# Performance work log

Hardware: AMD Instinct MI355X
Metric: run time of the kernel (lower is better)

The kernel has to match this reference:

```python
import jax, jax.numpy as jnp
import numpy as np

B, S, D_DIM = 32, 512, 1024

def setup_inputs() -> dict:
    key = jax.random.key(0)
    k1, k2, k3, k4 = jax.random.split(key, 4)
    return {
        "D": jax.random.normal(k1, (B, S, D_DIM), dtype=jnp.float32),
        "H": jax.random.normal(k2, (B, S, D_DIM), dtype=jnp.float32),
        # learned params: U is (d+1, d) (xavier-style scale), W is (2d+1,)
        # (original inits W to zeros; we use small random values so the linear
        #  term is exercised — same math either way)
        "U": jax.random.normal(k3, (D_DIM + 1, D_DIM), dtype=jnp.float32) * 0.02,
        "W": jax.random.normal(k4, (2 * D_DIM + 1,), dtype=jnp.float32) * 0.02,
    }

def reference(D, H, U, W):
    # D, H: [B, S, d]; U: [d+1, d]; W: [2d+1]
    d = H.shape[-1]
    ones = jnp.ones(D.shape[:2] + (1,), dtype=D.dtype)
    Daug = jnp.concatenate([D, ones], axis=-1)              # [B, S, d+1]
    # bilinear term: v.U.u  -> [B, Sx, Sy]
    bil = jnp.einsum('bxi,ij,byj->bxy', Daug, U, H)
    # linear term W . concat(D_aug, H): algebraically split — avoids the
    # O(B*S*S*2d) concatenated intermediate of the original implementation
    lin = (Daug @ W[:d + 1])[:, :, None] + (H @ W[d + 1:])[:, None, :]
    return bil + lin
```

## Files before the change

kernel.cpp:

```cpp
#include <hip/hip_runtime.h>


#define D_DIM 1024
#define ROWS 16384

typedef float floatx4 __attribute__((ext_vector_type(4)));
typedef __bf16 bf16x8 __attribute__((ext_vector_type(8)));
typedef __bf16 bf16x4 __attribute__((ext_vector_type(4)));

__device__ inline unsigned short f2bf(float f) {
  unsigned int u = __builtin_bit_cast(unsigned int, f);
  u = (u + 0x7FFFu + ((u >> 16) & 1u)) >> 16;
  return (unsigned short)u;
}

__device__ inline void async_load16(const void* g, void* l) {
  __builtin_amdgcn_global_load_lds(
      (const __attribute__((address_space(1))) void*)g,
      (__attribute__((address_space(3))) void*)l, 16, 0, 0);
}

__global__ __launch_bounds__(256) void transU_kernel(
    const float* __restrict__ U, const float* __restrict__ W,
    unsigned short* __restrict__ Ut, float* __restrict__ Wh) {
  if (blockIdx.x == 0 && blockIdx.y == 0) {
    #pragma unroll
    for (int i = 0; i < 4; ++i)
      Wh[threadIdx.x + 256 * i] = W[D_DIM + 1 + threadIdx.x + 256 * i];
  }
  __shared__ float tile[32][33];
  int n0 = blockIdx.x * 32;
  int k0 = blockIdx.y * 32;
  int t = threadIdx.x;
  int tr = t >> 5, tc = t & 31;
  #pragma unroll
  for (int i = 0; i < 32; i += 8)
    tile[tr + i][tc] = U[(size_t)(k0 + tr + i) * D_DIM + n0 + tc];
  __syncthreads();
  #pragma unroll
  for (int i = 0; i < 32; i += 8)
    Ut[(size_t)(n0 + tr + i) * D_DIM + k0 + tc] = f2bf(tile[tc][tr + i]);
}

template <bool F32_IS_A>
__device__ inline void gemm_core_mixed(
    const unsigned short* __restrict__ Ga,
    const float* __restrict__ Gf,
    bool do_lin, const float* WvS,
    float (&part)[8],
    unsigned short* As, unsigned short* Bs,
    floatx4 (&acc)[4][4]) {
  const int K = D_DIM;
  int tid = threadIdx.x;
  int l = tid & 63, wave = tid >> 6;
  int quad = l >> 4, lrow = l & 15;
  int wm = wave >> 1, wn = wave & 1;

  unsigned short* Sasync = F32_IS_A ? Bs : As;
  unsigned short* Sf32   = F32_IS_A ? As : Bs;

  int srow = 8 * wave + (l >> 3);
  int sq = (l & 7) ^ (l >> 3);
  const unsigned short* gasync = Ga + (size_t)srow * K + sq * 8;

  int rl = lrow & 7, gofs = lrow >> 3;
  int baseA = wm * 512 + gofs * 64 + rl * 8;
  int baseB = wn * 512 + gofs * 64 + rl * 8;

  int qi = tid & 15, frow = tid >> 4;
  const float* gf = Gf + (size_t)frow * K + qi * 4;
  int half = qi & 1, q = qi >> 1;
  int cofs[8];
  #pragma unroll
  for (int i = 0; i < 8; ++i) {
    int row = 16 * i + frow;
    cofs[i] = ((row >> 3) * 64 + (row & 7) * 8 + (q ^ (row & 7))) * 8 + half * 4;
  }

  float4 vc[8], vn[8];
  #pragma unroll
  for (int i = 0; i < 8; ++i)
    vc[i] = *(const float4*)(gf + (size_t)(16 * i) * K);

  for (int k0 = 0; k0 < K; k0 += 64) {
    asm volatile("" ::: "memory");
    __builtin_amdgcn_s_barrier();
    asm volatile("" ::: "memory");
    #pragma unroll
    for (int j = 0; j < 4; ++j)
      async_load16(gasync + (size_t)(32 * j) * K + k0, Sasync + (j * 256 + tid) * 8);
    __builtin_amdgcn_sched_barrier(0);
    int kn = (k0 + 64 < K) ? (k0 + 64) : k0;
    #pragma unroll
    for (int i = 0; i < 8; ++i)
      vn[i] = *(const float4*)(gf + (size_t)(16 * i) * K + kn);
    if (do_lin) {
      float4 wq = *(const float4*)&WvS[k0 + qi * 4];
      #pragma unroll
      for (int i = 0; i < 8; ++i)
        part[i] += vc[i].x * wq.x + vc[i].y * wq.y + vc[i].z * wq.z + vc[i].w * wq.w;
    }
    #pragma unroll
    for (int i = 0; i < 8; ++i) {
      bf16x4 o = { (__bf16)vc[i].x, (__bf16)vc[i].y, (__bf16)vc[i].z, (__bf16)vc[i].w };
      *(bf16x4*)(Sf32 + cofs[i]) = o;
    }
    asm volatile("s_waitcnt vmcnt(8) lgkmcnt(0)" ::: "memory");
    __builtin_amdgcn_sched_barrier(0);
    __builtin_amdgcn_s_barrier();
    asm volatile("" ::: "memory");
    #pragma unroll
    for (int s = 0; s < 2; ++s) {
      int xq = (s * 4 + quad) ^ rl;
      bf16x8 a[4], b[4];
      #pragma unroll
      for (int mt = 0; mt < 4; ++mt)
        a[mt] = *(const bf16x8*)(As + (baseA + mt * 128 + xq) * 8);
      #pragma unroll
      for (int nt = 0; nt < 4; ++nt)
        b[nt] = *(const bf16x8*)(Bs + (baseB + nt * 128 + xq) * 8);
      #pragma unroll
      for (int mt = 0; mt < 4; ++mt)
        #pragma unroll
        for (int nt = 0; nt < 4; ++nt)
          acc[mt][nt] = __builtin_amdgcn_mfma_f32_16x16x32_bf16(
              a[mt], b[nt], acc[mt][nt], 0, 0, 0);
    }
    #pragma unroll
    for (int i = 0; i < 8; ++i) vc[i] = vn[i];
  }
  #pragma unroll
  for (int i = 0; i < 8; ++i)
    asm volatile("" :: "v"(vc[i].x));
}

__global__ __launch_bounds__(256) void gemm1_kernel(
    const float* __restrict__ Df,
    const unsigned short* __restrict__ Ut,
    const float* __restrict__ Ubias,
    const float* __restrict__ W,
    unsigned short* __restrict__ T,
    float* __restrict__ linD) {
  __shared__ __align__(16) unsigned short As[128 * 64];
  __shared__ __align__(16) unsigned short Bs[128 * 64];
  __shared__ float WvS[1024];
  int m0 = blockIdx.x * 128, n0 = blockIdx.y * 128;
  int tid = threadIdx.x;
  int lane = tid & 63, wave = tid >> 6;
  int quad = lane >> 4, lrow = lane & 15;
  int wm = wave >> 1, wn = wave & 1;
  bool do_lin = (blockIdx.y == 0);

  ((float4*)WvS)[tid] = ((const float4*)W)[tid];
  __syncthreads();

  float part[8] = {};
  floatx4 acc[4][4] = {};
  gemm_core_mixed<true>(Ut + (size_t)n0 * D_DIM, Df + (size_t)m0 * D_DIM,
                        do_lin, WvS, part, As, Bs, acc);

  #pragma unroll
  for (int mt = 0; mt < 4; ++mt)
    #pragma unroll
    for (int nt = 0; nt < 4; ++nt) {
      int row = m0 + wm * 64 + mt * 16 + quad * 4;
      int col = n0 + wn * 64 + nt * 16 + lrow;
      float bias = Ubias[col];
      #pragma unroll
      for (int rr = 0; rr < 4; ++rr)
        T[(size_t)(row + rr) * D_DIM + col] = f2bf(acc[mt][nt][rr] + bias);
    }

  if (do_lin) {
    __syncthreads();
    float* red = (float*)As;
    #pragma unroll
    for (int i = 0; i < 8; ++i)
      red[(16 * i + (tid >> 4)) * 16 + (tid & 15)] = part[i];
    __syncthreads();
    if (tid < 128) {
      float s = 0.f;
      #pragma unroll
      for (int j = 0; j < 16; ++j) s += red[tid * 16 + j];
      linD[m0 + tid] = s + W[D_DIM];
    }
  }
}

__global__ __launch_bounds__(256) void gemm2_kernel(
    const unsigned short* __restrict__ Tg,
    const float* __restrict__ Hf,
    const float* __restrict__ Wh,
    const float* __restrict__ linD,
    float* __restrict__ out) {
  __shared__ __align__(16) unsigned short As[128 * 64];
  __shared__ __align__(16) unsigned short Bs[128 * 64];
  __shared__ float WvS[1024];
  __shared__ float linh_s[128];
  int b = blockIdx.x;
  int t = blockIdx.y;
  int m0 = (t >> 2) * 128, n0 = (t & 3) * 128;
  int tid = threadIdx.x;
  int lane = tid & 63, wave = tid >> 6;
  int quad = lane >> 4, lrow = lane & 15;
  int wm = wave >> 1, wn = wave & 1;

  ((float4*)WvS)[tid] = ((const float4*)Wh)[tid];
  __syncthreads();

  float part[8] = {};
  floatx4 acc[4][4] = {};
  gemm_core_mixed<false>(Tg + ((size_t)b * 512 + m0) * D_DIM,
                         Hf + ((size_t)b * 512 + n0) * D_DIM,
                         true, WvS, part, As, Bs, acc);

  __syncthreads();
  float* red = (float*)Bs;
  #pragma unroll
  for (int i = 0; i < 8; ++i)
    red[(16 * i + (tid >> 4)) * 16 + (tid & 15)] = part[i];
  __syncthreads();
  if (tid < 128) {
    float s = 0.f;
    #pragma unroll
    for (int j = 0; j < 16; ++j) s += red[tid * 16 + j];
    linh_s[tid] = s;
  }
  __syncthreads();

  #pragma unroll
  for (int mt = 0; mt < 4; ++mt)
    #pragma unroll
    for (int nt = 0; nt < 4; ++nt) {
      int row = m0 + wm * 64 + mt * 16 + quad * 4;
      int col = n0 + wn * 64 + nt * 16 + lrow;
      float lh = linh_s[wn * 64 + nt * 16 + lrow];
      #pragma unroll
      for (int rr = 0; rr < 4; ++rr) {
        float v = acc[mt][nt][rr] + linD[b * 512 + row + rr] + lh;
        out[((size_t)b * 512 + row + rr) * 512 + col] = v;
      }
    }
}

extern "C" void kernel_launch(void* const* d_in, const int* in_sizes, int n_in,
                              void* d_out, int out_size, void* d_ws, size_t ws_size,
                              hipStream_t stream) {
  const float* D = (const float*)d_in[0];
  const float* H = (const float*)d_in[1];
  const float* U = (const float*)d_in[2];
  const float* W = (const float*)d_in[3];
  float* out = (float*)d_out;

  char* ws = (char*)d_ws;
  unsigned short* Tbf = (unsigned short*)ws; ws += (size_t)ROWS * D_DIM * 2;
  unsigned short* Ut  = (unsigned short*)ws; ws += (size_t)D_DIM * D_DIM * 2;
  float* linD = (float*)ws;                  ws += (size_t)ROWS * 4;
  float* Wh   = (float*)ws;                  ws += (size_t)D_DIM * 4;

  transU_kernel<<<dim3(32, 32), 256, 0, stream>>>(U, W, Ut, Wh);
  gemm1_kernel<<<dim3(128, 8), 256, 0, stream>>>(D, Ut, U + (size_t)D_DIM * D_DIM, W, Tbf, linD);
  gemm2_kernel<<<dim3(32, 16), 256, 0, stream>>>(Tbf, H, Wh, linD, out);
}
```

Before: 224.1 us.

## Double-buffer async bf16 operand tiles in LDS to prefetch a full stage ahead

Adds a second LDS buffer for the async-loaded bf16 operand and unrolls the K loop by two with a macro, so the direct-to-LDS load for the next tile is issued into the other buffer while the current one is consumed. The wait changes from vmcnt(8) before the barrier to vmcnt(12) before the f32 conversion, letting the async loads stay in flight across a whole iteration. The cost is 16KB more LDS per block, which may reduce occupancy, and more register pressure from the unrolled body.

```diff
diff --git a/kernel.cpp b/kernel.cpp
--- a/kernel.cpp
+++ b/kernel.cpp
@@ -48,7 +48,7 @@
     const float* __restrict__ Gf,
     bool do_lin, const float* WvS,
     float (&part)[8],
-    unsigned short* As, unsigned short* Bs,
+    unsigned short* Sf32, unsigned short* Sa0, unsigned short* Sa1,
     floatx4 (&acc)[4][4]) {
   const int K = D_DIM;
   int tid = threadIdx.x;
@@ -56,9 +56,6 @@
   int quad = l >> 4, lrow = l & 15;
   int wm = wave >> 1, wn = wave & 1;
 
-  unsigned short* Sasync = F32_IS_A ? Bs : As;
-  unsigned short* Sf32   = F32_IS_A ? As : Bs;
-
   int srow = 8 * wave + (l >> 3);
   int sq = (l & 7) ^ (l >> 3);
   const unsigned short* gasync = Ga + (size_t)srow * K + sq * 8;
@@ -77,61 +74,82 @@
     cofs[i] = ((row >> 3) * 64 + (row & 7) * 8 + (q ^ (row & 7))) * 8 + half * 4;
   }
 
-  float4 vc[8], vn[8];
+  float4 vA[8], vB[8];
+  #pragma unroll
+  for (int j = 0; j < 4; ++j)
+    async_load16(gasync + (size_t)(32 * j) * K, Sa0 + (j * 256 + tid) * 8);
+  __builtin_amdgcn_sched_barrier(0);
   #pragma unroll
   for (int i = 0; i < 8; ++i)
-    vc[i] = *(const float4*)(gf + (size_t)(16 * i) * K);
-
-  for (int k0 = 0; k0 < K; k0 += 64) {
-    asm volatile("" ::: "memory");
-    __builtin_amdgcn_s_barrier();
-    asm volatile("" ::: "memory");
-    #pragma unroll
-    for (int j = 0; j < 4; ++j)
-      async_load16(gasync + (size_t)(32 * j) * K + k0, Sasync + (j * 256 + tid) * 8);
-    __builtin_amdgcn_sched_barrier(0);
-    int kn = (k0 + 64 < K) ? (k0 + 64) : k0;
-    #pragma unroll
-    for (int i = 0; i < 8; ++i)
-      vn[i] = *(const float4*)(gf + (size_t)(16 * i) * K + kn);
-    if (do_lin) {
-      float4 wq = *(const float4*)&WvS[k0 + qi * 4];
-      #pragma unroll
-      for (int i = 0; i < 8; ++i)
-        part[i] += vc[i].x * wq.x + vc[i].y * wq.y + vc[i].z * wq.z + vc[i].w * wq.w;
-    }
-    #pragma unroll
-    for (int i = 0; i < 8; ++i) {
-      bf16x4 o = { (__bf16)vc[i].x, (__bf16)vc[i].y, (__bf16)vc[i].z, (__bf16)vc[i].w };
-      *(bf16x4*)(Sf32 + cofs[i]) = o;
-    }
-    asm volatile("s_waitcnt vmcnt(8) lgkmcnt(0)" ::: "memory");
-    __builtin_amdgcn_sched_barrier(0);
-    __builtin_amdgcn_s_barrier();
-    asm volatile("" ::: "memory");
-    #pragma unroll
-    for (int s = 0; s < 2; ++s) {
-      int xq = (s * 4 + quad) ^ rl;
-      bf16x8 a[4], b[4];
-      #pragma unroll
-      for (int mt = 0; mt < 4; ++mt)
-        a[mt] = *(const bf16x8*)(As + (baseA + mt * 128 + xq) * 8);
-      #pragma unroll
-      for (int nt = 0; nt < 4; ++nt)
-        b[nt] = *(const bf16x8*)(Bs + (baseB + nt * 128 + xq) * 8);
-      #pragma unroll
-      for (int mt = 0; mt < 4; ++mt)
-        #pragma unroll
-        for (int nt = 0; nt < 4; ++nt)
-          acc[mt][nt] = __builtin_amdgcn_mfma_f32_16x16x32_bf16(
-              a[mt], b[nt], acc[mt][nt], 0, 0, 0);
-    }
-    #pragma unroll
-    for (int i = 0; i < 8; ++i) vc[i] = vn[i];
-  }
+    vA[i] = *(const float4*)(gf + (size_t)(16 * i) * K);
+  __builtin_amdgcn_sched_barrier(0);
+
+#define TILE_BODY(K0, KN, VCUR, VNXT, SCUR, SNXT)                              \
+  {                                                                            \
+    asm volatile("" ::: "memory");                                             \
+    __builtin_amdgcn_s_barrier();               \
+    asm volatile("" ::: "memory");                                             \
+    _Pragma("unroll")                                                          \
+    for (int j = 0; j < 4; ++j)                                                \
+      async_load16(gasync + (size_t)(32 * j) * K + (KN),                       \
+                   (SNXT) + (j * 256 + tid) * 8);                              \
+    __builtin_amdgcn_sched_barrier(0);                                         \
+    _Pragma("unroll")                                                          \
+    for (int i = 0; i < 8; ++i)                                                \
+      (VNXT)[i] = *(const float4*)(gf + (size_t)(16 * i) * K + (KN));          \
+    __builtin_amdgcn_sched_barrier(0);                                         \
+      \
+    asm volatile("s_waitcnt vmcnt(12)" ::: "memory");                          \
+    __builtin_amdgcn_sched_barrier(0);                                         \
+    if (do_lin) {                                                              \
+      float4 wq = *(const float4*)&WvS[(K0) + qi * 4];                         \
+      _Pragma("unroll")                                                        \
+      for (int i = 0; i < 8; ++i)                                              \
+        part[i] += (VCUR)[i].x * wq.x + (VCUR)[i].y * wq.y +                   \
+                   (VCUR)[i].z * wq.z + (VCUR)[i].w * wq.w;                    \
+    }                                                                          \
+    _Pragma("unroll")                                                          \
+    for (int i = 0; i < 8; ++i) {                                              \
+      bf16x4 o = { (__bf16)(VCUR)[i].x, (__bf16)(VCUR)[i].y,                   \
+                   (__bf16)(VCUR)[i].z, (__bf16)(VCUR)[i].w };                 \
+      *(bf16x4*)(Sf32 + cofs[i]) = o;           \
+    }                                                                          \
+    asm volatile("s_waitcnt lgkmcnt(0)" ::: "memory");                         \
+    __builtin_amdgcn_sched_barrier(0);                                         \
+    __builtin_amdgcn_s_barrier();                       \
+    asm volatile("" ::: "memory");                                             \
+    const unsigned short* Ap = F32_IS_A ? Sf32 : (SCUR);                       \
+    const unsigned short* Bp = F32_IS_A ? (SCUR) : Sf32;                       \
+    _Pragma("unroll")                                                          \
+    for (int s = 0; s < 2; ++s) {                                              \
+      int xq = (s * 4 + quad) ^ rl;                                            \
+      bf16x8 a[4], b[4];                                                       \
+      _Pragma("unroll")                                                        \
+      for (int mt = 0; mt < 4; ++mt)                                           \
+        a[mt] = *(const bf16x8*)(Ap + (baseA + mt * 128 + xq) * 8);            \
+      _Pragma("unroll")                                                        \
+      for (int nt = 0; nt < 4; ++nt)                                           \
+        b[nt] = *(const bf16x8*)(Bp + (baseB + nt * 128 + xq) * 8);            \
+      _Pragma("unroll")                                                        \
+      for (int mt = 0; mt < 4; ++mt)                                           \
+        _Pragma("unroll")                                                      \
+        for (int nt = 0; nt < 4; ++nt)                                         \
+          acc[mt][nt] = __builtin_amdgcn_mfma_f32_16x16x32_bf16(               \
+              a[mt], b[nt], acc[mt][nt], 0, 0, 0);                             \
+    }                                                                          \
+  }
+
+  for (int di = 0; di < 8; ++di) {
+    int k0 = di * 128;
+    int knb = (k0 + 128 < K) ? (k0 + 128) : (K - 64);
+    TILE_BODY(k0,      k0 + 64, vA, vB, Sa0, Sa1);
+    TILE_BODY(k0 + 64, knb,     vB, vA, Sa1, Sa0);
+  }
+#undef TILE_BODY
+
   #pragma unroll
   for (int i = 0; i < 8; ++i)
-    asm volatile("" :: "v"(vc[i].x));
+    asm volatile("" :: "v"(vA[i].x), "v"(vA[i].y), "v"(vA[i].z), "v"(vA[i].w));
 }
 
 __global__ __launch_bounds__(256) void gemm1_kernel(
@@ -141,8 +159,9 @@
     const float* __restrict__ W,
     unsigned short* __restrict__ T,
     float* __restrict__ linD) {
-  __shared__ __align__(16) unsigned short As[128 * 64];
-  __shared__ __align__(16) unsigned short Bs[128 * 64];
+  __shared__ __align__(16) unsigned short Sf32[128 * 64];
+  __shared__ __align__(16) unsigned short Sa0[128 * 64];
+  __shared__ __align__(16) unsigned short Sa1[128 * 64];
   __shared__ float WvS[1024];
   int m0 = blockIdx.x * 128, n0 = blockIdx.y * 128;
   int tid = threadIdx.x;
@@ -157,7 +176,7 @@
   float part[8] = {};
   floatx4 acc[4][4] = {};
   gemm_core_mixed<true>(Ut + (size_t)n0 * D_DIM, Df + (size_t)m0 * D_DIM,
-                        do_lin, WvS, part, As, Bs, acc);
+                        do_lin, WvS, part, Sf32, Sa0, Sa1, acc);
 
   #pragma unroll
   for (int mt = 0; mt < 4; ++mt)
@@ -173,7 +192,7 @@
 
   if (do_lin) {
     __syncthreads();
-    float* red = (float*)As;
+    float* red = (float*)Sf32;
     #pragma unroll
     for (int i = 0; i < 8; ++i)
       red[(16 * i + (tid >> 4)) * 16 + (tid & 15)] = part[i];
@@ -193,8 +212,9 @@
     const float* __restrict__ Wh,
     const float* __restrict__ linD,
     float* __restrict__ out) {
-  __shared__ __align__(16) unsigned short As[128 * 64];
-  __shared__ __align__(16) unsigned short Bs[128 * 64];
+  __shared__ __align__(16) unsigned short Sf32[128 * 64];
+  __shared__ __align__(16) unsigned short Sa0[128 * 64];
+  __shared__ __align__(16) unsigned short Sa1[128 * 64];
   __shared__ float WvS[1024];
   __shared__ float linh_s[128];
   int b = blockIdx.x;
@@ -212,10 +232,10 @@
   floatx4 acc[4][4] = {};
   gemm_core_mixed<false>(Tg + ((size_t)b * 512 + m0) * D_DIM,
                          Hf + ((size_t)b * 512 + n0) * D_DIM,
-                         true, WvS, part, As, Bs, acc);
-
-  __syncthreads();
-  float* red = (float*)Bs;
+                         true, WvS, part, Sf32, Sa0, Sa1, acc);
+
+  __syncthreads();
+  float* red = (float*)Sa0;
   #pragma unroll
   for (int i = 0; i < 8; ++i)
     red[(16 * i + (tid >> 4)) * 16 + (tid & 15)] = part[i];
```

New measurement: 245.1 us. 9.4% more time.
